# Kernel tuning notes

Hardware: AMD Instinct MI355X
Metric: run time of the kernel (lower is better)

## Reference

```python
import jax, jax.numpy as jnp
import numpy as np

VOCAB = 32000
N = 4096        # reservoir_size
D = 32          # avg nonzeros per row -> density D/N
R_OUT = 512
BATCH = 8
T = 256
NNZ = N * D     # W_rec nonzeros = N*N*(D/N)


def setup_inputs() -> dict:
    key = jax.random.key(0)
    ks = jax.random.split(key, 9)
    x = jax.random.randint(ks[0], (BATCH, T), 0, VOCAB)
    # dense input table; sparse.mm(W_in_T, one_hot) == row gather W_in[x_t]
    W_in = jax.random.normal(ks[1], (VOCAB, N), jnp.float32)
    rec_rows = jax.random.randint(ks[2], (NNZ,), 0, N, dtype=jnp.int32)
    rec_cols = jax.random.randint(ks[3], (NNZ,), 0, N, dtype=jnp.int32)
    # small scale stands in for spectral-radius normalization (init-time detail)
    rec_vals = jax.random.normal(ks[4], (NNZ,), jnp.float32) * 0.05
    a = jax.random.uniform(ks[5], (N,), jnp.float32)  # leak rates in [0,1)
    B_w = jax.random.normal(ks[6], (R_OUT, N), jnp.float32) / np.sqrt(N)
    A_w = jax.random.normal(ks[7], (VOCAB, R_OUT), jnp.float32) / np.sqrt(R_OUT)
    A_b = jnp.zeros((VOCAB,), jnp.float32)
    return dict(x=x, W_in=W_in, rec_rows=rec_rows, rec_cols=rec_cols,
                rec_vals=rec_vals, a=a, B_w=B_w, A_w=A_w, A_b=A_b)


def reference(x, W_in, rec_rows, rec_cols, rec_vals, a, B_w, A_w, A_b):
    B = x.shape[0]

    def step(h, x_t):
        # input projection: one-hot @ W_in  ==  row gather
        u = W_in[x_t]                                   # (B, N)
        # sparse COO matvec: rec = W_rec @ h^T, batched over B
        contrib = rec_vals[None, :] * h[:, rec_cols]    # (B, nnz)
        rec = jnp.zeros_like(h).at[:, rec_rows].add(contrib)
        pre = jnp.clip(u + rec, -10.0, 10.0)
        h_new = (1.0 - a) * h + a * jnp.tanh(pre)
        out = (h_new @ B_w.T) @ A_w.T + A_b             # (B, vocab)
        return h_new, out

    h0 = jnp.zeros((B, W_in.shape[1]), W_in.dtype)
    _, outs = jax.lax.scan(step, h0, x.T)               # (T, B, V)
    return jnp.transpose(outs, (1, 0, 2))               # (B, T, V)
```

## Files before the change

### kernel.cpp

```cpp
#include <hip/hip_runtime.h>
#include <hip/hip_bf16.h>
#include <stdint.h>

#define N_RES 4096
#define BATCH 8
#define T_STEPS 256
#define VOCAB 32000
#define R_OUT 512
#define NNZ 131072
#define NNZ_CAP 163840
#define TEAMS 8
#define SLICES 16
#define ROWS_PS 256
#define NWG (TEAMS*SLICES)
#define CSR_CAP 10240

typedef _Float16 v8h __attribute__((ext_vector_type(8)));
typedef float v4f __attribute__((ext_vector_type(4)));

static __device__ __forceinline__ unsigned short f2h(float f) {
    _Float16 h = (_Float16)f;
    unsigned short u;
    __builtin_memcpy(&u, &h, 2);
    return u;
}
static __device__ __forceinline__ float h2f(unsigned short u) {
    _Float16 h;
    __builtin_memcpy(&h, &u, 2);
    return (float)h;
}


#define FLAG_WORDS (TEAMS * SLICES * 32)
#define INIT_WORDS (NNZ_CAP + 4096 + FLAG_WORDS)

__global__ __launch_bounds__(256) void k_init(unsigned* __restrict__ csr,
                                              int* __restrict__ cnt,
                                              unsigned* __restrict__ flags) {
    int i = blockIdx.x * 256 + threadIdx.x;
    if (i < NNZ_CAP) csr[i] = 0u;
    else if (i < NNZ_CAP + 4096) cnt[i - NNZ_CAP] = 0;
    else if (i < INIT_WORDS) flags[i - NNZ_CAP - 4096] = 0u;
}


__global__ __launch_bounds__(256) void k_hist(const int* __restrict__ rows,
                                              int* __restrict__ cnt) {
    int i = blockIdx.x * 256 + threadIdx.x;
    if (i < NNZ) atomicAdd(&cnt[rows[i]], 1);
}

__global__ __launch_bounds__(1024) void k_scan(const int* __restrict__ cnt,
                                               int* __restrict__ row_ptr,
                                               int* __restrict__ cursor) {
    __shared__ int sm[1024];
    int t = threadIdx.x;
    int base = t * 4;
    int c0 = (cnt[base] + 7) & ~7;
    int c1 = (cnt[base + 1] + 7) & ~7;
    int c2 = (cnt[base + 2] + 7) & ~7;
    int c3 = (cnt[base + 3] + 7) & ~7;
    int s = c0 + c1 + c2 + c3;
    sm[t] = s;
    __syncthreads();
    for (int off = 1; off < 1024; off <<= 1) {
        int v = (t >= off) ? sm[t - off] : 0;
        __syncthreads();
        sm[t] += v;
        __syncthreads();
    }
    int run = sm[t] - s;
    row_ptr[base] = run;     cursor[base] = run;     run += c0;
    row_ptr[base + 1] = run; cursor[base + 1] = run; run += c1;
    row_ptr[base + 2] = run; cursor[base + 2] = run; run += c2;
    row_ptr[base + 3] = run; cursor[base + 3] = run; run += c3;
    if (t == 1023) row_ptr[4096] = run;
}

__global__ __launch_bounds__(256) void k_fill(const int* __restrict__ rows,
                                              const int* __restrict__ cols,
                                              const float* __restrict__ vals,
                                              int* __restrict__ cursor,
                                              unsigned* __restrict__ csr) {
    int i = blockIdx.x * 256 + threadIdx.x;
    if (i < NNZ) {
        int r = rows[i];
        int c = cols[i];
        int p = atomicAdd(&cursor[r], 1);
        unsigned off = ((unsigned)(c & 15) << 10) | ((unsigned)(c >> 4) << 2);
        csr[p] = (off << 16) | (unsigned)f2h(vals[i]);
    }
}


#define NB8 (R_OUT * N_RES / 8)
#define NA8 (VOCAB * R_OUT / 8)

__global__ __launch_bounds__(256) void k_cvt2(const float* __restrict__ Bw,
                                              unsigned short* __restrict__ Bwh,
                                              const float* __restrict__ Aw,
                                              unsigned short* __restrict__ Awh) {
    int i = blockIdx.x * 256 + threadIdx.x;
    const float* src;
    unsigned short* dst;
    int j;
    if (i < NB8) { src = Bw; dst = Bwh; j = i * 8; }
    else if (i < NB8 + NA8) { src = Aw; dst = Awh; j = (i - NB8) * 8; }
    else return;
    float4 a0 = *reinterpret_cast<const float4*>(src + j);
    float4 a1 = *reinterpret_cast<const float4*>(src + j + 4);
    unsigned short o[8] = { f2h(a0.x), f2h(a0.y), f2h(a0.z), f2h(a0.w),
                            f2h(a1.x), f2h(a1.y), f2h(a1.z), f2h(a1.w) };
    *reinterpret_cast<uint4*>(dst + j) = *reinterpret_cast<const uint4*>(o);
}


__global__ __launch_bounds__(256) void k_steps(const int* __restrict__ rowptr,
                                               const unsigned* __restrict__ csr,
                                               const float* __restrict__ W_in,
                                               const int* __restrict__ x,
                                               const float* __restrict__ a,
                                               unsigned short* __restrict__ Hb,
                                               unsigned long long* __restrict__ hx,
                                               unsigned* __restrict__ flags) {
    __shared__ float plane[4096];
    __shared__ __align__(16) unsigned lcsr[CSR_CAP];
    __shared__ unsigned long long stage64[64];
    __shared__ int ltok[T_STEPS];

    int wg = blockIdx.x;
    int tid = threadIdx.x;
    int team = wg & 7;
    int slice = wg >> 3;
    int r_own = slice * ROWS_PS + tid;

    ltok[tid] = x[team * T_STEPS + tid];

    int j0 = rowptr[slice * ROWS_PS];
    int j1 = rowptr[slice * ROWS_PS + ROWS_PS];
    int cntE = j1 - j0;
    if (cntE > CSR_CAP) cntE = CSR_CAP;
    {
        const uint4* src = reinterpret_cast<const uint4*>(csr + j0);
        int n4 = cntE >> 2;
        for (int k = tid; k < n4; k += 256)
            reinterpret_cast<uint4*>(lcsr)[k] = src[k];
    }
    for (int k = tid; k < 4096; k += 256) plane[k] = 0.f;

    int js = rowptr[r_own] - j0;
    int je = rowptr[r_own + 1] - j0;
    if (js > CSR_CAP) js = CSR_CAP;
    if (je > CSR_CAP) je = CSR_CAP;
    float av = a[r_own];
    float oma = 1.f - av;
    int pown = ((r_own & 15) << 8) | (r_own >> 4);
    __syncthreads();

    float u_cur = W_in[(size_t)ltok[0] * N_RES + r_own];

    for (int t = 0; t < T_STEPS; ++t) {
        float u_nxt = 0.f;
        if (t + 1 < T_STEPS)
            u_nxt = W_in[(size_t)ltok[t + 1] * N_RES + r_own];

        float acc = 0.f;
        for (int j = js; j < je; j += 8) {
            uint4 e0 = *reinterpret_cast<const uint4*>(lcsr + j);
            uint4 e1 = *reinterpret_cast<const uint4*>(lcsr + j + 4);
            unsigned ee[8] = { e0.x, e0.y, e0.z, e0.w, e1.x, e1.y, e1.z, e1.w };
#pragma unroll
            for (int q = 0; q < 8; ++q) {
                float g = *reinterpret_cast<const float*>(
                    reinterpret_cast<const char*>(plane) + (ee[q] >> 16));
                acc += h2f((unsigned short)(ee[q] & 0xffffu)) * g;
            }
        }
        float hold = plane[pown];
        float pre = u_cur + acc;
        pre = fminf(fmaxf(pre, -10.f), 10.f);
        float ex = __expf(2.f * pre);
        float th = 1.f - 2.f / (ex + 1.f);
        float hv = oma * hold + av * th;
        unsigned short hv16 = f2h(hv);
        Hb[((size_t)(team * T_STEPS + t) << 12) + r_own] = hv16;
        u_cur = u_nxt;

        if (t == T_STEPS - 1) break;

        reinterpret_cast<unsigned short*>(stage64)[tid] = hv16;
        __syncthreads();
        int par = t & 1;
        unsigned long long* base = hx + ((size_t)(par * TEAMS + team)) * 1024;
        if (tid < 64) {
            unsigned long long d = stage64[tid];
            __hip_atomic_store(base + slice * 64 + tid, d,
                               __ATOMIC_RELAXED, __HIP_MEMORY_SCOPE_AGENT);
        }
        asm volatile("s_waitcnt vmcnt(0)" ::: "memory");
        __syncthreads();
        if (tid == 0)
            __hip_atomic_store(flags + (team * SLICES + slice) * 32, (unsigned)(t + 1),
                               __ATOMIC_RELAXED, __HIP_MEMORY_SCOPE_AGENT);
        if (tid < SLICES) {
            const unsigned* fp = flags + (team * SLICES + tid) * 32;
            while (__hip_atomic_load(fp, __ATOMIC_RELAXED,
                                     __HIP_MEMORY_SCOPE_AGENT) < (unsigned)(t + 1)) {}
        }
        __syncthreads();
        const unsigned long long* src = base + tid * 4;
#pragma unroll
        for (int k = 0; k < 4; ++k) {
            unsigned long long d = __hip_atomic_load(src + k, __ATOMIC_RELAXED,
                                                     __HIP_MEMORY_SCOPE_AGENT);
            int jb = k * 4;
            plane[((jb + 0) << 8) | tid] = h2f((unsigned short)(d & 0xffffu));
            plane[((jb + 1) << 8) | tid] = h2f((unsigned short)((d >> 16) & 0xffffu));
            plane[((jb + 2) << 8) | tid] = h2f((unsigned short)((d >> 32) & 0xffffu));
            plane[((jb + 3) << 8) | tid] = h2f((unsigned short)((d >> 48) & 0xffffu));
        }
        __syncthreads();
    }
}


__global__ __launch_bounds__(512) void k_gemm1(const unsigned short* __restrict__ Hb,
                                               const unsigned short* __restrict__ Bwh,
                                               unsigned short* __restrict__ Rbh) {
    int lane = threadIdx.x & 63, wave = threadIdx.x >> 6;
    int wm = wave >> 1, wn = wave & 1;
    int row0 = blockIdx.y * 128;
    int col0 = blockIdx.x * 128 + wn * 64;
    int rA = lane & 15, kA = (lane >> 4) * 8;
    v4f acc[2][4];
    for (int s = 0; s < 2; ++s)
        for (int f = 0; f < 4; ++f)
            acc[s][f] = (v4f){0.f, 0.f, 0.f, 0.f};

    for (int k0 = 0; k0 < N_RES; k0 += 32) {
        v8h af[2];
#pragma unroll
        for (int s = 0; s < 2; ++s) {
            int r = row0 + (wm * 2 + s) * 16 + rA;
            af[s] = *reinterpret_cast<const v8h*>(Hb + (size_t)r * N_RES + k0 + kA);
        }
        v8h bf[4];
#pragma unroll
        for (int f = 0; f < 4; ++f) {
            int c = col0 + f * 16 + rA;
            bf[f] = *reinterpret_cast<const v8h*>(Bwh + (size_t)c * N_RES + k0 + kA);
        }
#pragma unroll
        for (int s = 0; s < 2; ++s)
#pragma unroll
            for (int f = 0; f < 4; ++f)
                acc[s][f] = __builtin_amdgcn_mfma_f32_16x16x32_f16(af[s], bf[f], acc[s][f], 0, 0, 0);
    }
#pragma unroll
    for (int s = 0; s < 2; ++s)
#pragma unroll
        for (int f = 0; f < 4; ++f) {
            int col = col0 + f * 16 + (lane & 15);
#pragma unroll
            for (int r = 0; r < 4; ++r) {
                int row = row0 + (wm * 2 + s) * 16 + (lane >> 4) * 4 + r;
                Rbh[(size_t)row * R_OUT + col] = f2h(acc[s][f][r]);
            }
        }
}


__global__ __launch_bounds__(512) void k_gemm2(const unsigned short* __restrict__ Rbh,
                                               const unsigned short* __restrict__ Awh,
                                               const float* __restrict__ Ab,
                                               float* __restrict__ out) {
    int lane = threadIdx.x & 63, wave = threadIdx.x >> 6;
    int wm = wave >> 1, wn = wave & 1;
    int row0 = blockIdx.x * 256;
    int col0 = blockIdx.y * 128 + wn * 64;
    int rA = lane & 15, kA = (lane >> 4) * 8;
    v4f acc[4][4];
    for (int s = 0; s < 4; ++s)
        for (int f = 0; f < 4; ++f)
            acc[s][f] = (v4f){0.f, 0.f, 0.f, 0.f};

    for (int k0 = 0; k0 < R_OUT; k0 += 32) {
        v8h af[4];
#pragma unroll
        for (int s = 0; s < 4; ++s) {
            int r = row0 + (wm * 4 + s) * 16 + rA;
            af[s] = *reinterpret_cast<const v8h*>(Rbh + (size_t)r * R_OUT + k0 + kA);
        }
        v8h bf[4];
#pragma unroll
        for (int f = 0; f < 4; ++f) {
            int c = col0 + f * 16 + rA;
            bf[f] = *reinterpret_cast<const v8h*>(Awh + (size_t)c * R_OUT + k0 + kA);
        }
#pragma unroll
        for (int s = 0; s < 4; ++s)
#pragma unroll
            for (int f = 0; f < 4; ++f)
                acc[s][f] = __builtin_amdgcn_mfma_f32_16x16x32_f16(af[s], bf[f], acc[s][f], 0, 0, 0);
    }
#pragma unroll
    for (int f = 0; f < 4; ++f) {
        int col = col0 + f * 16 + (lane & 15);
        float bias = Ab[col];
#pragma unroll
        for (int s = 0; s < 4; ++s) {
#pragma unroll
            for (int r = 0; r < 4; ++r) {
                int row = row0 + (wm * 4 + s) * 16 + (lane >> 4) * 4 + r;
                out[(size_t)row * VOCAB + col] = acc[s][f][r] + bias;
            }
        }
    }
}


extern "C" void kernel_launch(void* const* d_in, const int* in_sizes, int n_in,
                              void* d_out, int out_size, void* d_ws, size_t ws_size,
                              hipStream_t stream) {
    const int*   x        = (const int*)d_in[0];
    const float* W_in     = (const float*)d_in[1];
    const int*   rec_rows = (const int*)d_in[2];
    const int*   rec_cols = (const int*)d_in[3];
    const float* rec_vals = (const float*)d_in[4];
    const float* a        = (const float*)d_in[5];
    const float* B_w      = (const float*)d_in[6];
    const float* A_w      = (const float*)d_in[7];
    const float* A_b      = (const float*)d_in[8];
    float* out = (float*)d_out;

    char* w = (char*)d_ws;
    size_t off = 0;
    auto alloc = [&](size_t bytes) { void* p = w + off; off = (off + bytes + 255) & ~(size_t)255; return p; };

    unsigned short* Hb     = (unsigned short*)alloc((size_t)2048 * N_RES * 2);
    unsigned short* Rbh    = (unsigned short*)alloc((size_t)2048 * R_OUT * 2);
    unsigned short* Bwh    = (unsigned short*)alloc((size_t)R_OUT * N_RES * 2);
    unsigned short* Awh    = (unsigned short*)alloc((size_t)VOCAB * R_OUT * 2);
    unsigned*       csr    = (unsigned*)alloc((size_t)NNZ_CAP * 4);
    int*            rowptr = (int*)alloc(4097 * 4);
    int*            cnt    = (int*)alloc(4096 * 4);
    int*            cursor = (int*)alloc(4096 * 4);
    unsigned long long* hx = (unsigned long long*)alloc(2 * TEAMS * 1024 * 8);
    unsigned*       flags  = (unsigned*)alloc(FLAG_WORDS * 4);

    k_init<<<(INIT_WORDS + 255) / 256, 256, 0, stream>>>(csr, cnt, flags);

    k_hist<<<(NNZ + 255) / 256, 256, 0, stream>>>(rec_rows, cnt);
    k_scan<<<1, 1024, 0, stream>>>(cnt, rowptr, cursor);
    k_fill<<<(NNZ + 255) / 256, 256, 0, stream>>>(rec_rows, rec_cols, rec_vals, cursor, csr);

    k_cvt2<<<(NB8 + NA8 + 255) / 256, 256, 0, stream>>>(B_w, Bwh, A_w, Awh);

    k_steps<<<NWG, 256, 0, stream>>>(rowptr, csr, W_in, x, a, Hb, hx, flags);

    k_gemm1<<<dim3(R_OUT / 128, 2048 / 128), 512, 0, stream>>>(Hb, Bwh, Rbh);
    k_gemm2<<<dim3(2048 / 256, VOCAB / 128), 512, 0, stream>>>(Rbh, Awh, A_b, out);
}
```

Before: 1.503 ms.

## Stage GEMM tiles through LDS with double-buffered async loads and coalesced stores

Both output GEMMs now copy 128x32 fp16 tiles of A and B into shared memory with global_load_lds, double-buffered so the next K slice loads while MFMAs run on the current one. Block size drops to 256 threads, each wave covering a 64x64 sub-tile. This replaces direct per-lane global fragment loads that fetched the same data repeatedly. The large gemm2 output is staged through LDS so each thread writes contiguous float4 rows, giving coalesced stores to the 32000-wide logits. In exchange the kernels add barriers and vmcnt waits every iteration and use more LDS, which can limit occupancy.

```diff
diff --git a/kernel.cpp b/kernel.cpp
--- a/kernel.cpp
+++ b/kernel.cpp
@@ -224,79 +224,113 @@
 }
 
 
-__global__ __launch_bounds__(512) void k_gemm1(const unsigned short* __restrict__ Hb,
-                                               const unsigned short* __restrict__ Bwh,
+static __device__ __forceinline__ void stage128x32(const _Float16* __restrict__ g,
+                                                   int ld, int row0, int k0,
+                                                   _Float16* lds, int wave, int lane) {
+#pragma unroll
+    for (int q = 0; q < 2; ++q) {
+        int i = wave * 128 + q * 64 + lane;
+        const _Float16* src = g + (size_t)(row0 + (i >> 2)) * ld + k0 + (i & 3) * 8;
+        int loff = __builtin_amdgcn_readfirstlane((wave * 128 + q * 64) * 16);
+        __builtin_amdgcn_global_load_lds(
+            (const __attribute__((address_space(1))) void*)src,
+            (__attribute__((address_space(3))) void*)((char*)lds + loff),
+            16, 0, 0);
+    }
+}
+
+
+__global__ __launch_bounds__(256) void k_gemm1(const _Float16* __restrict__ Hb,
+                                               const _Float16* __restrict__ Bwh,
                                                unsigned short* __restrict__ Rbh) {
-    int lane = threadIdx.x & 63, wave = threadIdx.x >> 6;
+    __shared__ _Float16 As[2][128 * 32];
+    __shared__ _Float16 Bs[2][128 * 32];
+    int tid = threadIdx.x, lane = tid & 63, wave = tid >> 6;
     int wm = wave >> 1, wn = wave & 1;
+    int col0 = blockIdx.x * 128;
     int row0 = blockIdx.y * 128;
-    int col0 = blockIdx.x * 128 + wn * 64;
     int rA = lane & 15, kA = (lane >> 4) * 8;
-    v4f acc[2][4];
-    for (int s = 0; s < 2; ++s)
+    v4f acc[4][4];
+#pragma unroll
+    for (int s = 0; s < 4; ++s)
+#pragma unroll
+        for (int f = 0; f < 4; ++f) acc[s][f] = (v4f){0.f, 0.f, 0.f, 0.f};
+
+    stage128x32(Hb,  N_RES, row0, 0, As[0], wave, lane);
+    stage128x32(Bwh, N_RES, col0, 0, Bs[0], wave, lane);
+    const int NIT = N_RES / 32;
+    for (int it = 0; it < NIT; ++it) {
+        int cur = it & 1;
+        __syncthreads();
+        asm volatile("s_waitcnt vmcnt(0)" ::: "memory");
+        __syncthreads();
+        if (it + 1 < NIT) {
+            stage128x32(Hb,  N_RES, row0, (it + 1) * 32, As[cur ^ 1], wave, lane);
+            stage128x32(Bwh, N_RES, col0, (it + 1) * 32, Bs[cur ^ 1], wave, lane);
+        }
+        v8h af[4], bf[4];
+#pragma unroll
+        for (int s = 0; s < 4; ++s)
+            af[s] = *reinterpret_cast<const v8h*>(&As[cur][(wm * 64 + s * 16 + rA) * 32 + kA]);
+#pragma unroll
         for (int f = 0; f < 4; ++f)
-            acc[s][f] = (v4f){0.f, 0.f, 0.f, 0.f};
-
-    for (int k0 = 0; k0 < N_RES; k0 += 32) {
-        v8h af[2];
-#pragma unroll
-        for (int s = 0; s < 2; ++s) {
-            int r = row0 + (wm * 2 + s) * 16 + rA;
-            af[s] = *reinterpret_cast<const v8h*>(Hb + (size_t)r * N_RES + k0 + kA);
-        }
-        v8h bf[4];
-#pragma unroll
-        for (int f = 0; f < 4; ++f) {
-            int c = col0 + f * 16 + rA;
-            bf[f] = *reinterpret_cast<const v8h*>(Bwh + (size_t)c * N_RES + k0 + kA);
-        }
-#pragma unroll
-        for (int s = 0; s < 2; ++s)
+            bf[f] = *reinterpret_cast<const v8h*>(&Bs[cur][(wn * 64 + f * 16 + rA) * 32 + kA]);
+#pragma unroll
+        for (int s = 0; s < 4; ++s)
 #pragma unroll
             for (int f = 0; f < 4; ++f)
                 acc[s][f] = __builtin_amdgcn_mfma_f32_16x16x32_f16(af[s], bf[f], acc[s][f], 0, 0, 0);
     }
 #pragma unroll
-    for (int s = 0; s < 2; ++s)
-#pragma unroll
-        for (int f = 0; f < 4; ++f) {
-            int col = col0 + f * 16 + (lane & 15);
+    for (int f = 0; f < 4; ++f) {
+        int col = col0 + wn * 64 + f * 16 + (lane & 15);
+#pragma unroll
+        for (int s = 0; s < 4; ++s)
 #pragma unroll
             for (int r = 0; r < 4; ++r) {
-                int row = row0 + (wm * 2 + s) * 16 + (lane >> 4) * 4 + r;
+                int row = row0 + wm * 64 + s * 16 + (lane >> 4) * 4 + r;
                 Rbh[(size_t)row * R_OUT + col] = f2h(acc[s][f][r]);
             }
-        }
-}
-
-
-__global__ __launch_bounds__(512) void k_gemm2(const unsigned short* __restrict__ Rbh,
-                                               const unsigned short* __restrict__ Awh,
+    }
+}
+
+
+__global__ __launch_bounds__(256) void k_gemm2(const _Float16* __restrict__ Rbh,
+                                               const _Float16* __restrict__ Awh,
                                                const float* __restrict__ Ab,
                                                float* __restrict__ out) {
-    int lane = threadIdx.x & 63, wave = threadIdx.x >> 6;
+    __shared__ _Float16 As[2][128 * 32];
+    __shared__ _Float16 Bs[2][128 * 32];
+    int tid = threadIdx.x, lane = tid & 63, wave = tid >> 6;
     int wm = wave >> 1, wn = wave & 1;
-    int row0 = blockIdx.x * 256;
-    int col0 = blockIdx.y * 128 + wn * 64;
+    int col0 = blockIdx.x * 128;
+    int row0 = blockIdx.y * 128;
     int rA = lane & 15, kA = (lane >> 4) * 8;
     v4f acc[4][4];
+#pragma unroll
     for (int s = 0; s < 4; ++s)
+#pragma unroll
+        for (int f = 0; f < 4; ++f) acc[s][f] = (v4f){0.f, 0.f, 0.f, 0.f};
+
+    stage128x32(Rbh, R_OUT, row0, 0, As[0], wave, lane);
+    stage128x32(Awh, R_OUT, col0, 0, Bs[0], wave, lane);
+    const int NIT = R_OUT / 32;
+    for (int it = 0; it < NIT; ++it) {
+        int cur = it & 1;
+        __syncthreads();
+        asm volatile("s_waitcnt vmcnt(0)" ::: "memory");
+        __syncthreads();
+        if (it + 1 < NIT) {
+            stage128x32(Rbh, R_OUT, row0, (it + 1) * 32, As[cur ^ 1], wave, lane);
+            stage128x32(Awh, R_OUT, col0, (it + 1) * 32, Bs[cur ^ 1], wave, lane);
+        }
+        v8h af[4], bf[4];
+#pragma unroll
+        for (int s = 0; s < 4; ++s)
+            af[s] = *reinterpret_cast<const v8h*>(&As[cur][(wm * 64 + s * 16 + rA) * 32 + kA]);
+#pragma unroll
         for (int f = 0; f < 4; ++f)
-            acc[s][f] = (v4f){0.f, 0.f, 0.f, 0.f};
-
-    for (int k0 = 0; k0 < R_OUT; k0 += 32) {
-        v8h af[4];
-#pragma unroll
-        for (int s = 0; s < 4; ++s) {
-            int r = row0 + (wm * 4 + s) * 16 + rA;
-            af[s] = *reinterpret_cast<const v8h*>(Rbh + (size_t)r * R_OUT + k0 + kA);
-        }
-        v8h bf[4];
-#pragma unroll
-        for (int f = 0; f < 4; ++f) {
-            int c = col0 + f * 16 + rA;
-            bf[f] = *reinterpret_cast<const v8h*>(Awh + (size_t)c * R_OUT + k0 + kA);
-        }
+            bf[f] = *reinterpret_cast<const v8h*>(&Bs[cur][(wn * 64 + f * 16 + rA) * 32 + kA]);
 #pragma unroll
         for (int s = 0; s < 4; ++s)
 #pragma unroll
@@ -305,16 +339,34 @@
     }
 #pragma unroll
     for (int f = 0; f < 4; ++f) {
-        int col = col0 + f * 16 + (lane & 15);
-        float bias = Ab[col];
-#pragma unroll
-        for (int s = 0; s < 4; ++s) {
-#pragma unroll
-            for (int r = 0; r < 4; ++r) {
-                int row = row0 + (wm * 4 + s) * 16 + (lane >> 4) * 4 + r;
-                out[(size_t)row * VOCAB + col] = acc[s][f][r] + bias;
-            }
-        }
+        float bias = Ab[col0 + wn * 64 + f * 16 + (lane & 15)];
+#pragma unroll
+        for (int s = 0; s < 4; ++s)
+#pragma unroll
+            for (int r = 0; r < 4; ++r) acc[s][f][r] += bias;
+    }
+    float* Ct = (float*)As;
+#pragma unroll
+    for (int s = 0; s < 4; ++s) {
+        __syncthreads();
+#pragma unroll
+        for (int f = 0; f < 4; ++f) {
+            int lc = wn * 64 + f * 16 + (lane & 15);
+            int lr = wm * 16 + (lane >> 4) * 4;
+#pragma unroll
+            for (int r = 0; r < 4; ++r)
+                Ct[(lr + r) * 128 + lc] = acc[s][f][r];
+        }
+        __syncthreads();
+        int lr2 = tid >> 3;
+        int lc2 = (tid & 7) * 16;
+        int grow = row0 + (lr2 & 15) + (lr2 >> 4) * 64 + s * 16;
+        float* dst = out + (size_t)grow * VOCAB + col0 + lc2;
+        const float* srcl = &Ct[lr2 * 128 + lc2];
+#pragma unroll
+        for (int v = 0; v < 4; ++v)
+            *reinterpret_cast<float4*>(dst + v * 4) =
+                *reinterpret_cast<const float4*>(srcl + v * 4);
     }
 }
 
@@ -358,6 +410,8 @@
 
     k_steps<<<NWG, 256, 0, stream>>>(rowptr, csr, W_in, x, a, Hb, hx, flags);
 
-    k_gemm1<<<dim3(R_OUT / 128, 2048 / 128), 512, 0, stream>>>(Hb, Bwh, Rbh);
-    k_gemm2<<<dim3(2048 / 256, VOCAB / 128), 512, 0, stream>>>(Rbh, Awh, A_b, out);
-}
+    k_gemm1<<<dim3(R_OUT / 128, 2048 / 128), 256, 0, stream>>>(
+        (const _Float16*)Hb, (const _Float16*)Bwh, Rbh);
+    k_gemm2<<<dim3(VOCAB / 128, 2048 / 128), 256, 0, stream>>>(
+        (const _Float16*)Rbh, (const _Float16*)Awh, A_b, out);
+}
```

New measurement: 1.342 ms. 10.7% less time.
